# Performance work log

Measured on AMD Instinct MI355X. Metric: run time of the kernel, lower is better.

## Reference

```python
import jax, jax.numpy as jnp
import numpy as np
import math

B, T, DIM = 4, 4096, 1024
HID = int(DIM * 1.5)  # 1536
K = 4                  # conv kernel size
S = 16                 # num_slots
D = 384                # slot_dim


def setup_inputs() -> dict:
    key = jax.random.key(0)
    ks = jax.random.split(key, 16)
    inp = {
        "x": jax.random.normal(ks[0], (B, T, DIM), jnp.float32),
        "input_w": jax.random.normal(ks[1], (2 * HID, DIM), jnp.float32) * DIM ** -0.5,
        "conv_w": jax.random.normal(ks[2], (HID, K), jnp.float32) * K ** -0.5,
        "conv_b": jnp.zeros((HID,), jnp.float32),
        "gates_w": jax.random.normal(ks[3], (2 * HID, HID), jnp.float32) * HID ** -0.5,
        "gates_b": jnp.zeros((2 * HID,), jnp.float32),
        "forget_base": jnp.linspace(-4.323, -9.0, HID).astype(jnp.float32),
        "output_w": jax.random.normal(ks[4], (DIM, HID), jnp.float32) * HID ** -0.5,
        "memory_slots": jax.random.normal(ks[5], (S, D), jnp.float32) * 0.02,
        "wq_w": jax.random.normal(ks[6], (D, D), jnp.float32) * 0.02,
        "wk_w": jax.random.normal(ks[7], (D, HID), jnp.float32) * 0.02,
        "wv_w": jax.random.normal(ks[8], (D, HID), jnp.float32) * 0.02,
        "wg_w": jax.random.normal(ks[9], (1, HID), jnp.float32) * 0.02,
        "rq_w": jax.random.normal(ks[10], (D, HID), jnp.float32) * 0.02,
        "rk_w": jax.random.normal(ks[11], (D, D), jnp.float32) * 0.02,
        "rv_w": jax.random.normal(ks[12], (HID, D), jnp.float32) * 0.02,
    }
    return inp


def _causal_dwconv(x, w, b):
    # x: [B,T,H], w: [H,K], b: [H]; torch Conv1d(padding=K-1) then [:, :T] == causal
    xp = jnp.pad(x, ((0, 0), (K - 1, 0), (0, 0)))
    taps = jnp.stack([xp[:, j:j + T, :] for j in range(K)], axis=-1)  # [B,T,H,K]
    return jnp.einsum('bthk,hk->bth', taps, w) + b


def _scan(alpha, x):
    # h_t = alpha_t * h_{t-1} + x_t, elementwise over channels; along axis 1 (time)
    def combine(c1, c2):
        a1, b1 = c1
        a2, b2 = c2
        return a1 * a2, a2 * b1 + b2
    return jax.lax.associative_scan(combine, (alpha, x), axis=1)[1]


def reference(x, input_w, conv_w, conv_b, gates_w, gates_b, forget_base, output_w,
              memory_slots, wq_w, wk_w, wv_w, wg_w, rq_w, rk_w, rv_w):
    L = T // S  # segment length
    proj = x @ input_w.T                       # [B,T,2H]
    gate, xh = proj[..., :HID], proj[..., HID:]
    xh = _causal_dwconv(xh, conv_w, conv_b)    # [B,T,H]
    g = xh @ gates_w.T + gates_b               # [B,T,2H]
    forget, inp = g[..., :HID], g[..., HID:]
    alpha = jnp.exp(-8.0 * jax.nn.softplus(forget_base) * jax.nn.sigmoid(forget))
    xh = jnp.sqrt(1.0 - alpha ** 2 + 1e-6) * jax.nn.sigmoid(inp) * xh
    h = _scan(alpha, xh)                       # [B,T,H]
    xh = gate * jax.nn.sigmoid(gate) * xh      # silu-gated

    # ---- write_memory(xh) ----
    xseg = xh.reshape(B, S, L, HID)
    q = memory_slots @ wq_w.T                  # [S,D]
    kmat = jnp.einsum('bslh,dh->bsld', xseg, wk_w)
    vmat = jnp.einsum('bslh,dh->bsld', xseg, wv_w)
    qk = jnp.einsum('sd,bsld->bsl', q, kmat) / math.sqrt(D)
    attn = jax.nn.softmax(qk, axis=-1)
    mem = jnp.einsum('bsl,bsld->bsd', attn, vmat)  # [B,S,D]

    # ---- read_memory(gelu(xh)*h, mem) ----
    xr = jax.nn.gelu(xh, approximate=False) * h    # [B,T,H]
    rq = xr @ rq_w.T                               # [B,T,D]
    rk = mem @ rk_w.T                              # [B,S,D]
    rv = mem @ rv_w.T                              # [B,S,H]
    qk2 = jnp.einsum('btd,bsd->bts', rq, rk) / math.sqrt(D)
    seg = jnp.arange(T) // L
    mask = seg[:, None] <= jnp.arange(S)[None, :]  # [T,S]
    qk2 = jnp.where(mask[None], qk2, -jnp.inf)
    attn2 = jax.nn.softmax(qk2, axis=-1)
    out = jnp.einsum('bts,bsh->bth', attn2, rv)
    out = jax.nn.sigmoid(xr @ wg_w.T) * out        # write_gate on xr
    return out @ output_w.T                        # [B,T,DIM]
```

## Files before the change

### kernel.cpp

```cpp
#include <hip/hip_runtime.h>
#include <math.h>

#define BB 4
#define TT 4096
#define DIMW 1024
#define HID 1536
#define HID2 3072
#define KC 4
#define SSEG 16
#define LSEG 256
#define DD 384
#define NCH 64
#define CHL 64
#define TH  ((size_t)TT*(size_t)HID)

typedef _Float16 h8 __attribute__((ext_vector_type(8)));
typedef float f4 __attribute__((ext_vector_type(4)));

#define RSCL 4.8828125e-4f

__device__ __forceinline__ void hsplit(float a, _Float16& h0, _Float16& h1)
{
    _Float16 t = (_Float16)a;
    float tf = (float)t;
    if (fabsf(tf) < 6.103515625e-05f) { t = (_Float16)0.f; tf = 0.f; }
    h0 = t;
    h1 = (_Float16)((a - tf) * 2048.0f);
}

__device__ __forceinline__ void gl_lds16(const _Float16* g, _Float16* l)
{
    __builtin_amdgcn_global_load_lds(
        (const __attribute__((address_space(1))) unsigned int*)g,
        (__attribute__((address_space(3))) unsigned int*)l,
        16, 0, 0);
}

__global__ __launch_bounds__(256) void split2t(const float* __restrict__ src,
                                               _Float16* __restrict__ dst,
                                               int R, int Kd, size_t ps)
{
    __shared__ float tile[64][65];
    const int tid = threadIdx.x;
    const int bx = blockIdx.x;
    const int by = blockIdx.y;
    {
        const int lr = tid >> 2;
        const int lc = (tid & 3) * 16;
        const float* s = src + (size_t)(by * 64 + lr) * Kd + bx * 64 + lc;
#pragma unroll
        for (int e = 0; e < 16; e++) tile[lr][lc + e] = s[e];
    }
    __syncthreads();
    const int c = tid >> 5;
    const int r0 = tid & 31;
#pragma unroll
    for (int rr = 0; rr < 2; rr++) {
        const int r = r0 + rr * 32;
        h8 h0v, h1v;
#pragma unroll
        for (int e = 0; e < 8; e++) {
            _Float16 a0, a1;
            hsplit(tile[r][c * 8 + e], a0, a1);
            h0v[e] = a0; h1v[e] = a1;
        }
        const size_t didx = ((size_t)(bx * 8 + c) * R + by * 64 + r) * 8;
        *(h8*)(dst + didx) = h0v;
        *(h8*)(dst + ps + didx) = h1v;
    }
}

__global__ __launch_bounds__(256) void catkv_kernel(const float* __restrict__ wk,
                                                    const float* __restrict__ wv,
                                                    float* __restrict__ wkv)
{
    const int half = DD * HID;
    int i = blockIdx.x * 256 + threadIdx.x;
    if (i < half) wkv[i] = wk[i];
    else if (i < 2 * half) wkv[i] = wv[i - half];
}

template<int MODE, int TM, int TN, int WRN, int WCN>
__global__ __launch_bounds__(WRN * WCN * 64, 2) void gemm_mfma(
    const _Float16* __restrict__ Ap, size_t aps,
    const _Float16* __restrict__ Wp, size_t wps,
    float* __restrict__ C0, float* __restrict__ C1,
    const float* __restrict__ X,
    _Float16* __restrict__ OP, size_t ops,
    int M, int Nout, int Kd)
{
    constexpr int NWAVE = WRN * WCN;
    constexpr int WTM = TM / WRN, WTN = TN / WCN;
    constexpr int MI = WTM / 16, NI = WTN / 16;
    constexpr int API = TM / 16;
    constexpr int BPI = TN / 16;
    constexpr int ATOT = 2 * API;
    constexpr int NISS = ATOT + 2 * BPI;
    static_assert(NISS % NWAVE == 0, "issue count must divide waves");
    constexpr bool DUAL = (MI * NI <= 16);

    __shared__ _Float16 Als[2][2][TM * 32];
    __shared__ _Float16 Bls[2][2][TN * 32];

    const int tid = threadIdx.x;
    const int lane = tid & 63;
    const int wv = tid >> 6;
    const int wr = wv / WCN, wc = wv % WCN;
    const int lr = lane & 15, lg = lane >> 4;

    int bx = blockIdx.x, by = blockIdx.y;
    {
        const int gx = gridDim.x;
        const int nwg = gx * gridDim.y;
        if ((nwg & 7) == 0) {
            int wg = by * gx + bx;
            wg = (wg & 7) * (nwg >> 3) + (wg >> 3);
            bx = wg % gx; by = wg / gx;
        }
    }
    const int m0 = bx * TM, n0 = by * TN;

    f4 acc1[MI][NI], acc2[MI][NI];
#pragma unroll
    for (int i = 0; i < MI; i++)
#pragma unroll
        for (int j = 0; j < NI; j++) {
            acc1[i][j] = (f4){0.f, 0.f, 0.f, 0.f};
            if constexpr (DUAL) acc2[i][j] = (f4){0.f, 0.f, 0.f, 0.f};
        }

    auto stage = [&](int kq0, int buf) {
#pragma unroll
        for (int j = 0; j < NISS / NWAVE; j++) {
            const int i = j * NWAVE + wv;
            if (i < ATOT) {
                const int pl = i / API, s = i - pl * API;
                const int kc = (s * 64) / TM, r0 = (s * 64) % TM;
                const _Float16* g = Ap + pl * aps
                    + ((size_t)(kq0 + kc) * M + m0 + r0) * 8 + lane * 8;
                gl_lds16(g, &Als[buf][pl][(kc * TM + r0) * 8]);
            } else {
                const int jj = i - ATOT;
                const int pl = jj / BPI, s = jj - pl * BPI;
                const int kc = (s * 64) / TN, r0 = (s * 64) % TN;
                const _Float16* g = Wp + pl * wps
                    + ((size_t)(kq0 + kc) * Nout + n0 + r0) * 8 + lane * 8;
                gl_lds16(g, &Bls[buf][pl][(kc * TN + r0) * 8]);
            }
        }
    };

    stage(0, 0);
    __syncthreads();

    const int NS = Kd / 32;
    for (int t = 0; t < NS; t++) {
        const int buf = t & 1;
        if (t + 1 < NS) stage((t + 1) * 4, buf ^ 1);

        h8 af0[MI], af1[MI];
#pragma unroll
        for (int mi = 0; mi < MI; mi++) {
            const int arow = wr * WTM + mi * 16 + lr;
            af0[mi] = *(const h8*)&Als[buf][0][(lg * TM + arow) * 8];
            af1[mi] = *(const h8*)&Als[buf][1][(lg * TM + arow) * 8];
        }
#pragma unroll
        for (int ni = 0; ni < NI; ni++) {
            const int brow = wc * WTN + ni * 16 + lr;
            h8 b0 = *(const h8*)&Bls[buf][0][(lg * TN + brow) * 8];
            h8 b1 = *(const h8*)&Bls[buf][1][(lg * TN + brow) * 8];
#pragma unroll
            for (int mi = 0; mi < MI; mi++) {
                acc1[mi][ni] = __builtin_amdgcn_mfma_f32_16x16x32_f16(af0[mi], b0, acc1[mi][ni], 0, 0, 0);
                if constexpr (DUAL) {
                    acc2[mi][ni] = __builtin_amdgcn_mfma_f32_16x16x32_f16(af1[mi], b0, acc2[mi][ni], 0, 0, 0);
                    acc2[mi][ni] = __builtin_amdgcn_mfma_f32_16x16x32_f16(af0[mi], b1, acc2[mi][ni], 0, 0, 0);
                } else {
                    f4 tmp = (f4){0.f, 0.f, 0.f, 0.f};
                    tmp = __builtin_amdgcn_mfma_f32_16x16x32_f16(af1[mi], b0, tmp, 0, 0, 0);
                    tmp = __builtin_amdgcn_mfma_f32_16x16x32_f16(af0[mi], b1, tmp, 0, 0, 0);
                    acc1[mi][ni] = acc1[mi][ni] + tmp * RSCL;
                }
            }
        }
        __syncthreads();
    }

#pragma unroll
    for (int mi = 0; mi < MI; mi++) {
#pragma unroll
        for (int ni = 0; ni < NI; ni++) {
#pragma unroll
            for (int r = 0; r < 4; r++) {
                float v;
                if constexpr (DUAL) v = acc1[mi][ni][r] + acc2[mi][ni][r] * RSCL;
                else                v = acc1[mi][ni][r];
                const int m = m0 + wr * WTM + mi * 16 + lg * 4 + r;
                const int n = n0 + wc * WTN + ni * 16 + lr;
                if constexpr (MODE == 1) {
                    if (n < HID) C0[(size_t)m * HID + n] = v;
                    else         C1[(size_t)m * HID + (n - HID)] = v;
                } else if constexpr (MODE == 2) {
                    double g = (double)v;
                    float fv = (float)((g / (1.0 + exp(-g))) * (double)X[(size_t)m * Nout + n]);
                    C0[(size_t)m * Nout + n] = fv;
                    _Float16 a0, a1;
                    hsplit(fv, a0, a1);
                    const size_t didx = ((size_t)(n >> 3) * M + m) * 8 + (n & 7);
                    OP[didx] = a0;
                    OP[ops + didx] = a1;
                } else {
                    C0[(size_t)m * Nout + n] = v;
                }
            }
        }
    }
}

template<int MODE, int TM, int TN>
__global__ __launch_bounds__(256) void gemm32(const float* __restrict__ A,
                                              const float* __restrict__ W,
                                              float* __restrict__ C0,
                                              float* __restrict__ C1,
                                              const float* __restrict__ X,
                                              int M, int Nout, int Kd)
{
    constexpr int GM = TM / 64;
    constexpr int GN = TN / 64;
    constexpr int AF4 = TM * 4;
    constexpr int WF4 = TN * 4;
    constexpr int ALOOP = (AF4 + 255) / 256;
    constexpr int WLOOP = (WF4 + 255) / 256;

    __shared__ float As[16][TM];
    __shared__ float Bs[16][TN];

    const int tid = threadIdx.x;
    const int m0 = blockIdx.x * TM;
    const int n0 = blockIdx.y * TN;
    const int tx = tid & 15, ty = tid >> 4;

    float acc[GM * 4][GN * 4];
#pragma unroll
    for (int i = 0; i < GM * 4; i++)
#pragma unroll
        for (int j = 0; j < GN * 4; j++) acc[i][j] = 0.0f;

    float4 aReg[ALOOP], wReg[WLOOP];

    auto issueLoads = [&](int k0) {
#pragma unroll
        for (int u = 0; u < ALOOP; u++) {
            const int idx = tid + u * 256;
            float4 v = make_float4(0.f, 0.f, 0.f, 0.f);
            if (idx < AF4) {
                const int row = idx >> 2, kq = (idx & 3) * 4;
                const long ar = (long)(m0 + row);
                if (ar < M) v = *(const float4*)(A + ar * (long)Kd + (k0 + kq));
            }
            aReg[u] = v;
        }
#pragma unroll
        for (int u = 0; u < WLOOP; u++) {
            const int idx = tid + u * 256;
            float4 v = make_float4(0.f, 0.f, 0.f, 0.f);
            if (idx < WF4) {
                const int row = idx >> 2, kq = (idx & 3) * 4;
                const long wr = (long)(n0 + row);
                v = *(const float4*)(W + wr * (long)Kd + (k0 + kq));
            }
            wReg[u] = v;
        }
    };
    auto writeLDS = [&]() {
#pragma unroll
        for (int u = 0; u < ALOOP; u++) {
            const int idx = tid + u * 256;
            if (idx < AF4) {
                const int row = idx >> 2, kq = (idx & 3) * 4;
                As[kq + 0][row] = aReg[u].x;
                As[kq + 1][row] = aReg[u].y;
                As[kq + 2][row] = aReg[u].z;
                As[kq + 3][row] = aReg[u].w;
            }
        }
#pragma unroll
        for (int u = 0; u < WLOOP; u++) {
            const int idx = tid + u * 256;
            if (idx < WF4) {
                const int row = idx >> 2, kq = (idx & 3) * 4;
                Bs[kq + 0][row] = wReg[u].x;
                Bs[kq + 1][row] = wReg[u].y;
                Bs[kq + 2][row] = wReg[u].z;
                Bs[kq + 3][row] = wReg[u].w;
            }
        }
    };

    issueLoads(0);
    writeLDS();
    __syncthreads();

    const int NT = Kd / 16;
    for (int t = 0; t < NT; t++) {
        if (t + 1 < NT) issueLoads((t + 1) * 16);
#pragma unroll
        for (int k = 0; k < 16; k++) {
            float a[GM * 4], b[GN * 4];
#pragma unroll
            for (int g = 0; g < GM; g++) {
                const float4 t4 = *(const float4*)&As[k][g * 64 + ty * 4];
                a[g * 4 + 0] = t4.x; a[g * 4 + 1] = t4.y;
                a[g * 4 + 2] = t4.z; a[g * 4 + 3] = t4.w;
            }
#pragma unroll
            for (int g = 0; g < GN; g++) {
                const float4 t4 = *(const float4*)&Bs[k][g * 64 + tx * 4];
                b[g * 4 + 0] = t4.x; b[g * 4 + 1] = t4.y;
                b[g * 4 + 2] = t4.z; b[g * 4 + 3] = t4.w;
            }
#pragma unroll
            for (int i = 0; i < GM * 4; i++)
#pragma unroll
                for (int j = 0; j < GN * 4; j++) acc[i][j] += a[i] * b[j];
        }
        __syncthreads();
        if (t + 1 < NT) {
            writeLDS();
            __syncthreads();
        }
    }

#pragma unroll
    for (int i = 0; i < GM * 4; i++) {
        const int m = m0 + (i >> 2) * 64 + ty * 4 + (i & 3);
        if (m >= M) continue;
#pragma unroll
        for (int j = 0; j < GN * 4; j++) {
            const int n = n0 + (j >> 2) * 64 + tx * 4 + (j & 3);
            if (n >= Nout) continue;
            C0[(long)m * Nout + n] = acc[i][j];
        }
    }
}

__global__ __launch_bounds__(256) void spb_kernel(const float* __restrict__ fb,
                                                  double* __restrict__ spb)
{
    int h = blockIdx.x * 256 + threadIdx.x;
    if (h < HID) {
        double xv = (double)fb[h];
        spb[h] = log1p(exp(xv));
    }
}

__global__ __launch_bounds__(256) void conv_kernel(const float* __restrict__ xin,
                                                   const float* __restrict__ cw,
                                                   const float* __restrict__ cb,
                                                   float* __restrict__ outp,
                                                   _Float16* __restrict__ outP,
                                                   size_t ps)
{
    size_t i = (size_t)blockIdx.x * 256 + threadIdx.x;
    if (i >= TH) return;
    int h = (int)(i % HID);
    int t = (int)(i / HID);
    double acc = (double)cb[h];
#pragma unroll
    for (int j = 0; j < KC; j++) {
        int tt = t - (KC - 1) + j;
        if (tt >= 0) acc += (double)cw[h * KC + j] * (double)xin[(size_t)tt * HID + h];
    }
    float fv = (float)acc;
    outp[i] = fv;
    _Float16 a0, a1;
    hsplit(fv, a0, a1);
    const size_t didx = ((size_t)(h >> 3) * TT + t) * 8 + (h & 7);
    outP[didx] = a0;
    outP[ps + didx] = a1;
}

__global__ __launch_bounds__(256) void alpha_xh2_kernel(float* __restrict__ fg,
                                                        float* __restrict__ ip,
                                                        const float* __restrict__ xh1,
                                                        const double* __restrict__ spb,
                                                        const float* __restrict__ gb)
{
    size_t i = (size_t)blockIdx.x * 256 + threadIdx.x;
    if (i >= TH) return;
    int h = (int)(i % HID);
    double f  = (double)fg[i] + (double)gb[h];
    double g2 = (double)ip[i] + (double)gb[HID + h];
    double sigf = 1.0 / (1.0 + exp(-f));
    double alpha = exp(-8.0 * spb[h] * sigf);
    double s2 = sqrt(1.0 - alpha * alpha + 1e-6);
    double sigi = 1.0 / (1.0 + exp(-g2));
    double x1 = (double)xh1[i];
    fg[i] = (float)alpha;
    ip[i] = (float)(s2 * sigi * x1);
}

__global__ __launch_bounds__(256) void scan1_kernel(const float* __restrict__ alpha,
                                                    const float* __restrict__ xh2,
                                                    double* __restrict__ cA,
                                                    double* __restrict__ cB)
{
    int idx = blockIdx.x * 256 + threadIdx.x;
    if (idx >= NCH * HID) return;
    int h = idx % HID;
    int c = idx / HID;
    size_t base = (size_t)c * CHL * HID + h;
    double aP = 1.0, bV = 0.0;
    for (int i = 0; i < CHL; i++) {
        double a  = (double)alpha[base + (size_t)i * HID];
        double xv = (double)xh2 [base + (size_t)i * HID];
        bV = a * bV + xv;
        aP *= a;
    }
    size_t o = (size_t)c * HID + h;
    cA[o] = aP;
    cB[o] = bV;
}

__global__ __launch_bounds__(256) void scan2_kernel(const double* __restrict__ cA,
                                                    const double* __restrict__ cB,
                                                    double* __restrict__ cH0)
{
    int h = blockIdx.x * 256 + threadIdx.x;
    if (h >= HID) return;
    double carry = 0.0;
    for (int c = 0; c < NCH; c++) {
        size_t o = (size_t)c * HID + h;
        cH0[o] = carry;
        carry = cA[o] * carry + cB[o];
    }
}

__global__ __launch_bounds__(256) void scan3_kernel(const float* __restrict__ alpha,
                                                    const float* __restrict__ xh2,
                                                    const double* __restrict__ cH0,
                                                    float* __restrict__ hout)
{
    int idx = blockIdx.x * 256 + threadIdx.x;
    if (idx >= NCH * HID) return;
    int h = idx % HID;
    int c = idx / HID;
    size_t base = (size_t)c * CHL * HID + h;
    double hv = cH0[(size_t)c * HID + h];
    for (int i = 0; i < CHL; i++) {
        double a  = (double)alpha[base + (size_t)i * HID];
        double xv = (double)xh2 [base + (size_t)i * HID];
        hv = a * hv + xv;
        hout[base + (size_t)i * HID] = (float)hv;
    }
}

__global__ __launch_bounds__(256) void gelu_mul_kernel(float* __restrict__ xh3,
                                                       const float* __restrict__ hbuf,
                                                       _Float16* __restrict__ outP,
                                                       size_t ps)
{
    size_t i = (size_t)blockIdx.x * 256 + threadIdx.x;
    if (i >= TH) return;
    int h = (int)(i % HID);
    int t = (int)(i / HID);
    double x3 = (double)xh3[i];
    double ge = 0.5 * x3 * (1.0 + erf(x3 * 0.70710678118654752440));
    float fv = (float)(ge * (double)hbuf[i]);
    xh3[i] = fv;
    _Float16 a0, a1;
    hsplit(fv, a0, a1);
    const size_t didx = ((size_t)(h >> 3) * TT + t) * 8 + (h & 7);
    outP[didx] = a0;
    outP[ps + didx] = a1;
}

__global__ __launch_bounds__(256) void attn1_kernel(const float* __restrict__ kv,
                                                    const float* __restrict__ qbuf,
                                                    float* __restrict__ mem)
{
    const int s = blockIdx.x;
    const int l = threadIdx.x;
    const size_t row = (size_t)s * LSEG + l;
    const float* kr = kv + row * (2 * DD);
    const float* qs = qbuf + (size_t)s * DD;
    double acc = 0.0;
    for (int d = 0; d < DD; d++) acc += (double)qs[d] * (double)kr[d];
    double qk = acc / sqrt((double)DD);
    __shared__ double r1[256];
    __shared__ double sw[256];
    r1[l] = qk; __syncthreads();
    for (int off = 128; off > 0; off >>= 1) {
        if (l < off) r1[l] = fmax(r1[l], r1[l + off]);
        __syncthreads();
    }
    double m = r1[0]; __syncthreads();
    double e = exp(qk - m);
    r1[l] = e; __syncthreads();
    for (int off = 128; off > 0; off >>= 1) {
        if (l < off) r1[l] += r1[l + off];
        __syncthreads();
    }
    double denom = r1[0];
    sw[l] = e / denom; __syncthreads();
    const size_t vbase = (size_t)s * LSEG * (2 * DD) + DD;
    for (int d = l; d < DD; d += 256) {
        double a2 = 0.0;
        for (int ll = 0; ll < LSEG; ll++)
            a2 += sw[ll] * (double)kv[vbase + (size_t)ll * (2 * DD) + d];
        mem[(size_t)s * DD + d] = (float)a2;
    }
}

__global__ __launch_bounds__(256) void attn2_kernel(const float* __restrict__ rq,
                                                    const float* __restrict__ rk,
                                                    const float* __restrict__ rv,
                                                    const float* __restrict__ xr,
                                                    const float* __restrict__ wg,
                                                    _Float16* __restrict__ outP,
                                                    size_t ps)
{
    const int t = blockIdx.x;
    const int sigma = t >> 8;
    const int tid = threadIdx.x;
    __shared__ double sqk[16];
    __shared__ double red[256];
    __shared__ double sw[16];
    __shared__ double sgate;

    const float* rqn = rq + (size_t)t * DD;
    {
        int s = tid >> 4, j = tid & 15;
        const float* rks = rk + (size_t)s * DD;
        double part = 0.0;
        for (int d = j; d < DD; d += 16) part += (double)rqn[d] * (double)rks[d];
#pragma unroll
        for (int off = 8; off > 0; off >>= 1) part += __shfl_down(part, off, 16);
        if (j == 0) sqk[s] = part;
    }
    double gp = 0.0;
    const float* xrn = xr + (size_t)t * HID;
    for (int hh = tid; hh < HID; hh += 256) gp += (double)xrn[hh] * (double)wg[hh];
    red[tid] = gp; __syncthreads();
    for (int off = 128; off > 0; off >>= 1) {
        if (tid < off) red[tid] += red[tid + off];
        __syncthreads();
    }
    if (tid == 0) {
        const double inv = 1.0 / sqrt((double)DD);
        double m = -1e300;
        for (int ss = sigma; ss < 16; ss++) {
            double v = sqk[ss] * inv;
            sqk[ss] = v;
            if (v > m) m = v;
        }
        double sum = 0.0;
        for (int ss = sigma; ss < 16; ss++) {
            double e = exp(sqk[ss] - m);
            sw[ss] = e;
            sum += e;
        }
        double isum = 1.0 / sum;
        for (int ss = 0; ss < sigma; ss++) sw[ss] = 0.0;
        for (int ss = sigma; ss < 16; ss++) sw[ss] *= isum;
        sgate = 1.0 / (1.0 + exp(-red[0]));
    }
    __syncthreads();
    const double gte = sgate;
    for (int c = tid; c < HID / 8; c += 256) {
        double accv[8] = {0, 0, 0, 0, 0, 0, 0, 0};
        for (int ss = sigma; ss < 16; ss++) {
            const float* rvp = rv + (size_t)ss * HID + c * 8;
            double w = sw[ss];
#pragma unroll
            for (int e = 0; e < 8; e++) accv[e] += w * (double)rvp[e];
        }
        h8 h0v, h1v;
#pragma unroll
        for (int e = 0; e < 8; e++) {
            _Float16 a0, a1;
            hsplit((float)(gte * accv[e]), a0, a1);
            h0v[e] = a0; h1v[e] = a1;
        }
        const size_t didx = ((size_t)c * TT + t) * 8;
        *(h8*)(outP + didx) = h0v;
        *(h8*)(outP + ps + didx) = h1v;
    }
}

extern "C" void kernel_launch(void* const* d_in, const int* in_sizes, int n_in,
                              void* d_out, int out_size, void* d_ws, size_t ws_size,
                              hipStream_t stream)
{
    const float* x            = (const float*)d_in[0];
    const float* input_w      = (const float*)d_in[1];
    const float* conv_w       = (const float*)d_in[2];
    const float* conv_b       = (const float*)d_in[3];
    const float* gates_w      = (const float*)d_in[4];
    const float* gates_b      = (const float*)d_in[5];
    const float* forget_base  = (const float*)d_in[6];
    const float* output_w     = (const float*)d_in[7];
    const float* memory_slots = (const float*)d_in[8];
    const float* wq_w         = (const float*)d_in[9];
    const float* wk_w         = (const float*)d_in[10];
    const float* wv_w         = (const float*)d_in[11];
    const float* wg_w         = (const float*)d_in[12];
    const float* rq_w         = (const float*)d_in[13];
    const float* rk_w         = (const float*)d_in[14];
    const float* rv_w         = (const float*)d_in[15];
    float* out = (float*)d_out;

    double* spb  = (double*)d_ws;
    double* cA   = spb + HID;
    double* cB   = cA + (size_t)NCH * HID;
    double* cH0  = cB + (size_t)NCH * HID;
    float* slotA = (float*)(cH0 + (size_t)NCH * HID);
    float* slotB = slotA + TH;
    float* slotC = slotB + TH;
    float* qbuf   = slotC + TH;
    float* membuf = qbuf + (size_t)SSEG * DD;
    float* rkbuf  = membuf + (size_t)SSEG * DD;
    float* rvbuf  = rkbuf + (size_t)SSEG * DD;

    _Float16* base_h = (_Float16*)(rvbuf + (size_t)SSEG * HID);
    const size_t iwN  = (size_t)HID * DIMW;
    const size_t gwN  = (size_t)HID2 * HID;
    const size_t kvN  = (size_t)(2 * DD) * HID;
    const size_t rqN  = (size_t)DD * HID;
    const size_t owN  = (size_t)DIMW * HID;
    const size_t xbN  = (size_t)TT * DIMW;
    _Float16* iwlo = base_h;
    _Float16* iwhi = iwlo + 2 * iwN;
    _Float16* gwp  = iwhi + 2 * iwN;
    _Float16* wkvp = gwp  + 2 * gwN;
    _Float16* rqwp = wkvp + 2 * kvN;
    _Float16* owp  = rqwp + 2 * rqN;
    _Float16* xbP  = owp  + 2 * owN;
    _Float16* P1   = xbP  + 2 * xbN;

    dim3 blk(256);
    dim3 blk512(512);
    const int ewBlocks = (int)(TH / 256);

    spb_kernel<<<(HID + 255) / 256, blk, 0, stream>>>(forget_base, spb);
    catkv_kernel<<<(2 * DD * HID) / 256, blk, 0, stream>>>(wk_w, wv_w, slotA);
    split2t<<<dim3(DIMW / 64, HID / 64), blk, 0, stream>>>(input_w, iwlo, HID, DIMW, iwN);
    split2t<<<dim3(DIMW / 64, HID / 64), blk, 0, stream>>>(input_w + (size_t)HID * DIMW,
                                                           iwhi, HID, DIMW, iwN);
    split2t<<<dim3(HID / 64, HID2 / 64), blk, 0, stream>>>(gates_w, gwp, HID2, HID, gwN);
    split2t<<<dim3(HID / 64, (2 * DD) / 64), blk, 0, stream>>>(slotA, wkvp, 2 * DD, HID, kvN);
    split2t<<<dim3(HID / 64, DD / 64), blk, 0, stream>>>(rq_w, rqwp, DD, HID, rqN);
    split2t<<<dim3(HID / 64, DIMW / 64), blk, 0, stream>>>(output_w, owp, DIMW, HID, owN);
    gemm32<0, 64, 64><<<dim3(1, DD / 64), blk, 0, stream>>>(
        memory_slots, wq_w, qbuf, (float*)nullptr, (const float*)nullptr, SSEG, DD, DD);

    for (int b = 0; b < BB; b++) {
        const float* xb   = x   + (size_t)b * TT * DIMW;
        float*       outb = out + (size_t)b * TT * DIMW;

        split2t<<<dim3(DIMW / 64, TT / 64), blk, 0, stream>>>(xb, xbP, TT, DIMW, xbN);
        gemm_mfma<0, 256, 128, 4, 2><<<dim3(TT / 256, HID / 128), blk512, 0, stream>>>(
            xbP, xbN, iwhi, iwN, slotB, (float*)nullptr, (const float*)nullptr,
            (_Float16*)nullptr, 0, TT, HID, DIMW);
        conv_kernel<<<ewBlocks, blk, 0, stream>>>(slotB, conv_w, conv_b, slotC, P1, TH);
        gemm_mfma<1, 256, 256, 4, 2><<<dim3(TT / 256, HID2 / 256), blk512, 0, stream>>>(
            P1, TH, gwp, gwN, slotA, slotB, (const float*)nullptr,
            (_Float16*)nullptr, 0, TT, HID2, HID);
        alpha_xh2_kernel<<<ewBlocks, blk, 0, stream>>>(slotA, slotB, slotC, spb, gates_b);
        scan1_kernel<<<(NCH * HID) / 256, blk, 0, stream>>>(slotA, slotB, cA, cB);
        scan2_kernel<<<(HID + 255) / 256, blk, 0, stream>>>(cA, cB, cH0);
        scan3_kernel<<<(NCH * HID) / 256, blk, 0, stream>>>(slotA, slotB, cH0, slotC);
        gemm_mfma<2, 256, 128, 4, 2><<<dim3(TT / 256, HID / 128), blk512, 0, stream>>>(
            xbP, xbN, iwlo, iwN, slotA, (float*)nullptr, slotB, P1, TH, TT, HID, DIMW);
        gemm_mfma<0, 128, 128, 2, 2><<<dim3(TT / 128, (2 * DD) / 128), blk, 0, stream>>>(
            P1, TH, wkvp, kvN, slotB, (float*)nullptr, (const float*)nullptr,
            (_Float16*)nullptr, 0, TT, 2 * DD, HID);
        attn1_kernel<<<SSEG, blk, 0, stream>>>(slotB, qbuf, membuf);
        gelu_mul_kernel<<<ewBlocks, blk, 0, stream>>>(slotA, slotC, P1, TH);
        gemm_mfma<0, 128, 128, 2, 2><<<dim3(TT / 128, DD / 128), blk, 0, stream>>>(
            P1, TH, rqwp, rqN, slotB, (float*)nullptr, (const float*)nullptr,
            (_Float16*)nullptr, 0, TT, DD, HID);
        gemm32<0, 64, 64><<<dim3(1, DD / 64), blk, 0, stream>>>(
            membuf, rk_w, rkbuf, (float*)nullptr, (const float*)nullptr, SSEG, DD, DD);
        gemm32<0, 64, 64><<<dim3(1, HID / 64), blk, 0, stream>>>(
            membuf, rv_w, rvbuf, (float*)nullptr, (const float*)nullptr, SSEG, HID, DD);
        attn2_kernel<<<TT, blk, 0, stream>>>(slotB, rkbuf, rvbuf, slotA, wg_w, P1, TH);
        gemm_mfma<0, 128, 128, 2, 2><<<dim3(TT / 128, DIMW / 128), blk, 0, stream>>>(
            P1, TH, owp, owN, outb, (float*)nullptr, (const float*)nullptr,
            (_Float16*)nullptr, 0, TT, DIMW, HID);
    }
}
```

Measured before the change: 2.736 ms.

## Add triple-buffered pipelined MFMA GEMM and drop double precision in elementwise kernels

Adds a gemm_pipe kernel that keeps three LDS stages in flight and waits on vmcnt with a single barrier per K step, so global-to-LDS loads overlap MFMA work better. The input-projection, gates and silu-gate GEMMs switch to it with 128x192 tiles. The conv, gate activation, gelu and silu epilogues move from double to float math, removing slow FP64 operations. This costs more LDS for the third buffer and may slightly change numerical accuracy.

Measured after the change: 2.771 ms. Within noise of the previous version (+1.3%).

```diff
diff --git a/kernel.cpp b/kernel.cpp
--- a/kernel.cpp
+++ b/kernel.cpp
@@ -80,8 +80,8 @@
     else if (i < 2 * half) wkv[i] = wv[i - half];
 }
 
-template<int MODE, int TM, int TN, int WRN, int WCN>
-__global__ __launch_bounds__(WRN * WCN * 64, 2) void gemm_mfma(
+template<int MODE, int TM, int TN>
+__global__ __launch_bounds__(512, 2) void gemm_pipe(
     const _Float16* __restrict__ Ap, size_t aps,
     const _Float16* __restrict__ Wp, size_t wps,
     float* __restrict__ C0, float* __restrict__ C1,
@@ -89,23 +89,23 @@
     _Float16* __restrict__ OP, size_t ops,
     int M, int Nout, int Kd)
 {
-    constexpr int NWAVE = WRN * WCN;
-    constexpr int WTM = TM / WRN, WTN = TN / WCN;
+    constexpr int WTM = TM / 2, WTN = TN / 4;
     constexpr int MI = WTM / 16, NI = WTN / 16;
+    static_assert(MI * NI <= 16, "DUAL path only");
     constexpr int API = TM / 16;
     constexpr int BPI = TN / 16;
     constexpr int ATOT = 2 * API;
     constexpr int NISS = ATOT + 2 * BPI;
-    static_assert(NISS % NWAVE == 0, "issue count must divide waves");
-    constexpr bool DUAL = (MI * NI <= 16);
-
-    __shared__ _Float16 Als[2][2][TM * 32];
-    __shared__ _Float16 Bls[2][2][TN * 32];
+    static_assert(NISS % 8 == 0, "issues must divide 8 waves");
+    constexpr int PW = NISS / 8;
+
+    __shared__ _Float16 Als[3][2][TM * 32];
+    __shared__ _Float16 Bls[3][2][TN * 32];
 
     const int tid = threadIdx.x;
     const int lane = tid & 63;
     const int wv = tid >> 6;
-    const int wr = wv / WCN, wc = wv % WCN;
+    const int wr = wv >> 2, wc = wv & 3;
     const int lr = lane & 15, lg = lane >> 4;
 
     int bx = blockIdx.x, by = blockIdx.y;
@@ -126,38 +126,41 @@
 #pragma unroll
         for (int j = 0; j < NI; j++) {
             acc1[i][j] = (f4){0.f, 0.f, 0.f, 0.f};
-            if constexpr (DUAL) acc2[i][j] = (f4){0.f, 0.f, 0.f, 0.f};
-        }
-
-    auto stage = [&](int kq0, int buf) {
-#pragma unroll
-        for (int j = 0; j < NISS / NWAVE; j++) {
-            const int i = j * NWAVE + wv;
+            acc2[i][j] = (f4){0.f, 0.f, 0.f, 0.f};
+        }
+
+    auto stage = [&](int ts) {
+        const int kq0 = ts * 4;
+        const int buf = ts % 3;
+#pragma unroll
+        for (int j = 0; j < PW; j++) {
+            const int i = j * 8 + wv;
             if (i < ATOT) {
                 const int pl = i / API, s = i - pl * API;
                 const int kc = (s * 64) / TM, r0 = (s * 64) % TM;
-                const _Float16* g = Ap + pl * aps
-                    + ((size_t)(kq0 + kc) * M + m0 + r0) * 8 + lane * 8;
-                gl_lds16(g, &Als[buf][pl][(kc * TM + r0) * 8]);
+                gl_lds16(Ap + pl * aps + ((size_t)(kq0 + kc) * M + m0 + r0) * 8 + lane * 8,
+                         &Als[buf][pl][(kc * TM + r0) * 8]);
             } else {
                 const int jj = i - ATOT;
                 const int pl = jj / BPI, s = jj - pl * BPI;
                 const int kc = (s * 64) / TN, r0 = (s * 64) % TN;
-                const _Float16* g = Wp + pl * wps
-                    + ((size_t)(kq0 + kc) * Nout + n0 + r0) * 8 + lane * 8;
-                gl_lds16(g, &Bls[buf][pl][(kc * TN + r0) * 8]);
+                gl_lds16(Wp + pl * wps + ((size_t)(kq0 + kc) * Nout + n0 + r0) * 8 + lane * 8,
+                         &Bls[buf][pl][(kc * TN + r0) * 8]);
             }
         }
     };
 
-    stage(0, 0);
-    __syncthreads();
-
     const int NS = Kd / 32;
+    stage(0);
+    stage(1);
+
     for (int t = 0; t < NS; t++) {
-        const int buf = t & 1;
-        if (t + 1 < NS) stage((t + 1) * 4, buf ^ 1);
-
+        if (t + 1 < NS) asm volatile("s_waitcnt vmcnt(%0)" :: "i"(PW) : "memory");
+        else            asm volatile("s_waitcnt vmcnt(0)" ::: "memory");
+        __builtin_amdgcn_s_barrier();
+        if (t + 2 < NS) stage(t + 2);
+
+        const int buf = t % 3;
         h8 af0[MI], af1[MI];
 #pragma unroll
         for (int mi = 0; mi < MI; mi++) {
@@ -173,18 +176,10 @@
 #pragma unroll
             for (int mi = 0; mi < MI; mi++) {
                 acc1[mi][ni] = __builtin_amdgcn_mfma_f32_16x16x32_f16(af0[mi], b0, acc1[mi][ni], 0, 0, 0);
-                if constexpr (DUAL) {
-                    acc2[mi][ni] = __builtin_amdgcn_mfma_f32_16x16x32_f16(af1[mi], b0, acc2[mi][ni], 0, 0, 0);
-                    acc2[mi][ni] = __builtin_amdgcn_mfma_f32_16x16x32_f16(af0[mi], b1, acc2[mi][ni], 0, 0, 0);
-                } else {
-                    f4 tmp = (f4){0.f, 0.f, 0.f, 0.f};
-                    tmp = __builtin_amdgcn_mfma_f32_16x16x32_f16(af1[mi], b0, tmp, 0, 0, 0);
-                    tmp = __builtin_amdgcn_mfma_f32_16x16x32_f16(af0[mi], b1, tmp, 0, 0, 0);
-                    acc1[mi][ni] = acc1[mi][ni] + tmp * RSCL;
-                }
-            }
-        }
-        __syncthreads();
+                acc2[mi][ni] = __builtin_amdgcn_mfma_f32_16x16x32_f16(af1[mi], b0, acc2[mi][ni], 0, 0, 0);
+                acc2[mi][ni] = __builtin_amdgcn_mfma_f32_16x16x32_f16(af0[mi], b1, acc2[mi][ni], 0, 0, 0);
+            }
+        }
     }
 
 #pragma unroll
@@ -193,17 +188,15 @@
         for (int ni = 0; ni < NI; ni++) {
 #pragma unroll
             for (int r = 0; r < 4; r++) {
-                float v;
-                if constexpr (DUAL) v = acc1[mi][ni][r] + acc2[mi][ni][r] * RSCL;
-                else                v = acc1[mi][ni][r];
+                const float v = acc1[mi][ni][r] + acc2[mi][ni][r] * RSCL;
                 const int m = m0 + wr * WTM + mi * 16 + lg * 4 + r;
                 const int n = n0 + wc * WTN + ni * 16 + lr;
                 if constexpr (MODE == 1) {
                     if (n < HID) C0[(size_t)m * HID + n] = v;
                     else         C1[(size_t)m * HID + (n - HID)] = v;
                 } else if constexpr (MODE == 2) {
-                    double g = (double)v;
-                    float fv = (float)((g / (1.0 + exp(-g))) * (double)X[(size_t)m * Nout + n]);
+                    float g = v;
+                    float fv = (g / (1.0f + expf(-g))) * X[(size_t)m * Nout + n];
                     C0[(size_t)m * Nout + n] = fv;
                     _Float16 a0, a1;
                     hsplit(fv, a0, a1);
@@ -218,6 +211,133 @@
     }
 }
 
+template<int MODE, int TM, int TN, int WRN, int WCN>
+__global__ __launch_bounds__(WRN * WCN * 64, 2) void gemm_mfma(
+    const _Float16* __restrict__ Ap, size_t aps,
+    const _Float16* __restrict__ Wp, size_t wps,
+    float* __restrict__ C0, float* __restrict__ C1,
+    const float* __restrict__ X,
+    _Float16* __restrict__ OP, size_t ops,
+    int M, int Nout, int Kd)
+{
+    constexpr int NWAVE = WRN * WCN;
+    constexpr int WTM = TM / WRN, WTN = TN / WCN;
+    constexpr int MI = WTM / 16, NI = WTN / 16;
+    constexpr int API = TM / 16;
+    constexpr int BPI = TN / 16;
+    constexpr int ATOT = 2 * API;
+    constexpr int NISS = ATOT + 2 * BPI;
+    static_assert(NISS % NWAVE == 0, "issue count must divide waves");
+    static_assert(MI * NI <= 16, "DUAL only");
+
+    __shared__ _Float16 Als[2][2][TM * 32];
+    __shared__ _Float16 Bls[2][2][TN * 32];
+
+    const int tid = threadIdx.x;
+    const int lane = tid & 63;
+    const int wv = tid >> 6;
+    const int wr = wv / WCN, wc = wv % WCN;
+    const int lr = lane & 15, lg = lane >> 4;
+
+    int bx = blockIdx.x, by = blockIdx.y;
+    {
+        const int gx = gridDim.x;
+        const int nwg = gx * gridDim.y;
+        if ((nwg & 7) == 0) {
+            int wg = by * gx + bx;
+            wg = (wg & 7) * (nwg >> 3) + (wg >> 3);
+            bx = wg % gx; by = wg / gx;
+        }
+    }
+    const int m0 = bx * TM, n0 = by * TN;
+
+    f4 acc1[MI][NI], acc2[MI][NI];
+#pragma unroll
+    for (int i = 0; i < MI; i++)
+#pragma unroll
+        for (int j = 0; j < NI; j++) {
+            acc1[i][j] = (f4){0.f, 0.f, 0.f, 0.f};
+            acc2[i][j] = (f4){0.f, 0.f, 0.f, 0.f};
+        }
+
+    auto stage = [&](int kq0, int buf) {
+#pragma unroll
+        for (int j = 0; j < NISS / NWAVE; j++) {
+            const int i = j * NWAVE + wv;
+            if (i < ATOT) {
+                const int pl = i / API, s = i - pl * API;
+                const int kc = (s * 64) / TM, r0 = (s * 64) % TM;
+                gl_lds16(Ap + pl * aps + ((size_t)(kq0 + kc) * M + m0 + r0) * 8 + lane * 8,
+                         &Als[buf][pl][(kc * TM + r0) * 8]);
+            } else {
+                const int jj = i - ATOT;
+                const int pl = jj / BPI, s = jj - pl * BPI;
+                const int kc = (s * 64) / TN, r0 = (s * 64) % TN;
+                gl_lds16(Wp + pl * wps + ((size_t)(kq0 + kc) * Nout + n0 + r0) * 8 + lane * 8,
+                         &Bls[buf][pl][(kc * TN + r0) * 8]);
+            }
+        }
+    };
+
+    stage(0, 0);
+    __syncthreads();
+
+    const int NS = Kd / 32;
+    for (int t = 0; t < NS; t++) {
+        const int buf = t & 1;
+        if (t + 1 < NS) stage((t + 1) * 4, buf ^ 1);
+
+        h8 af0[MI], af1[MI];
+#pragma unroll
+        for (int mi = 0; mi < MI; mi++) {
+            const int arow = wr * WTM + mi * 16 + lr;
+            af0[mi] = *(const h8*)&Als[buf][0][(lg * TM + arow) * 8];
+            af1[mi] = *(const h8*)&Als[buf][1][(lg * TM + arow) * 8];
+        }
+#pragma unroll
+        for (int ni = 0; ni < NI; ni++) {
+            const int brow = wc * WTN + ni * 16 + lr;
+            h8 b0 = *(const h8*)&Bls[buf][0][(lg * TN + brow) * 8];
+            h8 b1 = *(const h8*)&Bls[buf][1][(lg * TN + brow) * 8];
+#pragma unroll
+            for (int mi = 0; mi < MI; mi++) {
+                acc1[mi][ni] = __builtin_amdgcn_mfma_f32_16x16x32_f16(af0[mi], b0, acc1[mi][ni], 0, 0, 0);
+                acc2[mi][ni] = __builtin_amdgcn_mfma_f32_16x16x32_f16(af1[mi], b0, acc2[mi][ni], 0, 0, 0);
+                acc2[mi][ni] = __builtin_amdgcn_mfma_f32_16x16x32_f16(af0[mi], b1, acc2[mi][ni], 0, 0, 0);
+            }
+        }
+        __syncthreads();
+    }
+
+#pragma unroll
+    for (int mi = 0; mi < MI; mi++) {
+#pragma unroll
+        for (int ni = 0; ni < NI; ni++) {
+#pragma unroll
+            for (int r = 0; r < 4; r++) {
+                const float v = acc1[mi][ni][r] + acc2[mi][ni][r] * RSCL;
+                const int m = m0 + wr * WTM + mi * 16 + lg * 4 + r;
+                const int n = n0 + wc * WTN + ni * 16 + lr;
+                if constexpr (MODE == 1) {
+                    if (n < HID) C0[(size_t)m * HID + n] = v;
+                    else         C1[(size_t)m * HID + (n - HID)] = v;
+                } else if constexpr (MODE == 2) {
+                    float g = v;
+                    float fv = (g / (1.0f + expf(-g))) * X[(size_t)m * Nout + n];
+                    C0[(size_t)m * Nout + n] = fv;
+                    _Float16 a0, a1;
+                    hsplit(fv, a0, a1);
+                    const size_t didx = ((size_t)(n >> 3) * M + m) * 8 + (n & 7);
+                    OP[didx] = a0;
+                    OP[ops + didx] = a1;
+                } else {
+                    C0[(size_t)m * Nout + n] = v;
+                }
+            }
+        }
+    }
+}
+
 template<int MODE, int TM, int TN>
 __global__ __launch_bounds__(256) void gemm32(const float* __restrict__ A,
                                               const float* __restrict__ W,
@@ -366,16 +486,15 @@
     if (i >= TH) return;
     int h = (int)(i % HID);
     int t = (int)(i / HID);
-    double acc = (double)cb[h];
+    float acc = cb[h];
 #pragma unroll
     for (int j = 0; j < KC; j++) {
         int tt = t - (KC - 1) + j;
-        if (tt >= 0) acc += (double)cw[h * KC + j] * (double)xin[(size_t)tt * HID + h];
-    }
-    float fv = (float)acc;
-    outp[i] = fv;
+        if (tt >= 0) acc = fmaf(cw[h * KC + j], xin[(size_t)tt * HID + h], acc);
+    }
+    outp[i] = acc;
     _Float16 a0, a1;
-    hsplit(fv, a0, a1);
+    hsplit(acc, a0, a1);
     const size_t didx = ((size_t)(h >> 3) * TT + t) * 8 + (h & 7);
     outP[didx] = a0;
     outP[ps + didx] = a1;
@@ -391,14 +510,13 @@
     if (i >= TH) return;
     int h = (int)(i % HID);
     double f  = (double)fg[i] + (double)gb[h];
-    double g2 = (double)ip[i] + (double)gb[HID + h];
+    float g2 = ip[i] + gb[HID + h];
     double sigf = 1.0 / (1.0 + exp(-f));
-    double alpha = exp(-8.0 * spb[h] * sigf);
-    double s2 = sqrt(1.0 - alpha * alpha + 1e-6);
-    double sigi = 1.0 / (1.0 + exp(-g2));
-    double x1 = (double)xh1[i];
-    fg[i] = (float)alpha;
-    ip[i] = (float)(s2 * sigi * x1);
+    float alpha = (float)exp(-8.0 * spb[h] * sigf);
+    float s2 = sqrtf(1.0f - alpha * alpha + 1e-6f);
+    float sigi = 1.0f / (1.0f + expf(-g2));
+    fg[i] = alpha;
+    ip[i] = s2 * sigi * xh1[i];
 }
 
 __global__ __launch_bounds__(256) void scan1_kernel(const float* __restrict__ alpha,
@@ -465,9 +583,9 @@
     if (i >= TH) return;
     int h = (int)(i % HID);
     int t = (int)(i / HID);
-    double x3 = (double)xh3[i];
-    double ge = 0.5 * x3 * (1.0 + erf(x3 * 0.70710678118654752440));
-    float fv = (float)(ge * (double)hbuf[i]);
+    float x3 = xh3[i];
+    float ge = 0.5f * x3 * (1.0f + erff(x3 * 0.70710678f));
+    float fv = ge * hbuf[i];
     xh3[i] = fv;
     _Float16 a0, a1;
     hsplit(fv, a0, a1);
@@ -660,18 +778,18 @@
         float*       outb = out + (size_t)b * TT * DIMW;
 
         split2t<<<dim3(DIMW / 64, TT / 64), blk, 0, stream>>>(xb, xbP, TT, DIMW, xbN);
-        gemm_mfma<0, 256, 128, 4, 2><<<dim3(TT / 256, HID / 128), blk512, 0, stream>>>(
+        gemm_pipe<0, 128, 192><<<dim3(TT / 128, HID / 192), blk512, 0, stream>>>(
             xbP, xbN, iwhi, iwN, slotB, (float*)nullptr, (const float*)nullptr,
             (_Float16*)nullptr, 0, TT, HID, DIMW);
         conv_kernel<<<ewBlocks, blk, 0, stream>>>(slotB, conv_w, conv_b, slotC, P1, TH);
-        gemm_mfma<1, 256, 256, 4, 2><<<dim3(TT / 256, HID2 / 256), blk512, 0, stream>>>(
+        gemm_pipe<1, 128, 192><<<dim3(TT / 128, HID2 / 192), blk512, 0, stream>>>(
             P1, TH, gwp, gwN, slotA, slotB, (const float*)nullptr,
             (_Float16*)nullptr, 0, TT, HID2, HID);
         alpha_xh2_kernel<<<ewBlocks, blk, 0, stream>>>(slotA, slotB, slotC, spb, gates_b);
         scan1_kernel<<<(NCH * HID) / 256, blk, 0, stream>>>(slotA, slotB, cA, cB);
         scan2_kernel<<<(HID + 255) / 256, blk, 0, stream>>>(cA, cB, cH0);
         scan3_kernel<<<(NCH * HID) / 256, blk, 0, stream>>>(slotA, slotB, cH0, slotC);
-        gemm_mfma<2, 256, 128, 4, 2><<<dim3(TT / 256, HID / 128), blk512, 0, stream>>>(
+        gemm_pipe<2, 128, 192><<<dim3(TT / 128, HID / 192), blk512, 0, stream>>>(
             xbP, xbN, iwlo, iwN, slotA, (float*)nullptr, slotB, P1, TH, TT, HID, DIMW);
         gemm_mfma<0, 128, 128, 2, 2><<<dim3(TT / 128, (2 * DD) / 128), blk, 0, stream>>>(
             P1, TH, wkvp, kvN, slotB, (float*)nullptr, (const float*)nullptr,
```
